# Kernel optimization log

Measured on AMD Instinct MI355X. Metric: run time of the kernel, lower is better.

The kernel has to match this reference:

```python
import jax, jax.numpy as jnp
import numpy as np

H = 256  # hidden size
I = 2    # input size / output size


def setup_inputs() -> dict:
    key = jax.random.key(0)
    ks = jax.random.split(key, 11)
    s1 = 1.0 / np.sqrt(H)
    u = lambda k, shape: jax.random.uniform(k, shape, jnp.float32, -s1, s1)
    return {
        "inputs": jax.random.normal(ks[0], (512, 256, I), jnp.float32),
        "W_ih1": u(ks[1], (4 * H, I)),
        "W_hh1": u(ks[2], (4 * H, H)),
        "b_ih1": u(ks[3], (4 * H,)),
        "b_hh1": u(ks[4], (4 * H,)),
        "W_ih2": u(ks[5], (4 * H, H)),
        "W_hh2": u(ks[6], (4 * H, H)),
        "b_ih2": u(ks[7], (4 * H,)),
        "b_hh2": u(ks[8], (4 * H,)),
        "W_lin": u(ks[9], (I, H)),
        "b_lin": u(ks[10], (I,)),
    }


def _lstm_cell(x, h, c, W_ih, W_hh, b_ih, b_hh):
    # PyTorch LSTMCell gate order: i, f, g, o
    gates = x @ W_ih.T + b_ih + h @ W_hh.T + b_hh  # (B, 4H)
    i, f, g, o = jnp.split(gates, 4, axis=-1)
    c_new = jax.nn.sigmoid(f) * c + jax.nn.sigmoid(i) * jnp.tanh(g)
    h_new = jax.nn.sigmoid(o) * jnp.tanh(c_new)
    return h_new, c_new


def reference(inputs, W_ih1, W_hh1, b_ih1, b_hh1, W_ih2, W_hh2, b_ih2, b_hh2,
              W_lin, b_lin):
    B = inputs.shape[0]
    xs = jnp.transpose(inputs, (1, 0, 2))  # (T, B, I)
    zeros = jnp.zeros((B, H), inputs.dtype)
    carry0 = (zeros, zeros, zeros, zeros)

    def step(carry, x_t):
        h1, c1, h2, c2 = carry
        # NOTE: the original clones/masks x_t into lstm_input_t but never
        # uses it — the cell consumes raw input_t, so we do the same.
        h1, c1 = _lstm_cell(x_t, h1, c1, W_ih1, W_hh1, b_ih1, b_hh1)
        h2, c2 = _lstm_cell(h1, h2, c2, W_ih2, W_hh2, b_ih2, b_hh2)
        y = h2 @ W_lin.T + b_lin  # (B, I)
        return (h1, c1, h2, c2), y

    _, ys = jax.lax.scan(step, carry0, xs)  # ys: (T, B, I)
    return jnp.transpose(ys, (1, 0, 2))  # (B, T, I)
```

## Files before the change

### kernel.cpp

```cpp
#include <hip/hip_runtime.h>


typedef float vf2 __attribute__((ext_vector_type(2)));
typedef float v4f __attribute__((ext_vector_type(4)));
typedef _Float16 vh4 __attribute__((ext_vector_type(4)));
typedef _Float16 vh8 __attribute__((ext_vector_type(8)));

#define NT 512
#define TSTEPS 256
#define NSF 160
#define NVPF 24
#define NLPF 8
#define FRB 1024
#define VPBASE (1280 * FRB)
#define LPBASE (1472 * FRB)
#define FS 393216

__global__ void prep_kernel(const float* __restrict__ W_ih1,
                            const float* __restrict__ W_hh1,
                            const float* __restrict__ b_ih1,
                            const float* __restrict__ b_hh1,
                            const float* __restrict__ W_ih2,
                            const float* __restrict__ W_hh2,
                            const float* __restrict__ b_ih2,
                            const float* __restrict__ b_hh2,
                            void* __restrict__ ws) {
    const int stride = gridDim.x * blockDim.x;
    const int idx = blockIdx.x * blockDim.x + threadIdx.x;
    _Float16* wh = (_Float16*)ws;
    float* wf = (float*)ws;
    for (int e = idx; e < 786432; e += stride) {
        int kb = e >> 9;
        int lane = (e & 511) >> 3, jj = e & 7;
        int w, rt, kt, m;
        if (kb < 1280) {
            w = kb / 160; int f = kb % 160;
            if (f < 64)       { m = 0; rt = f >> 3;        kt = f & 7; }
            else if (f < 128) { m = 1; rt = (f - 64) >> 3; kt = f & 7; }
            else {
                int q = f - 128; m = 2; rt = q >> 2; int pos = q & 3;
                kt = (pos == 0) ? 0 : (pos == 1) ? 4 : (pos == 2) ? 5 : 7;
            }
        } else if (kb < 1472) {
            int p2 = kb - 1280; w = p2 / 24; int p = p2 % 24;
            m = 2; rt = p / 3; kt = 1 + p % 3;
        } else {
            int k3 = kb - 1472; w = k3 >> 3; int q = k3 & 7;
            m = 2; rt = q; kt = 6;
        }
        int row = w * 128 + rt * 16 + (lane & 15);
        int k   = kt * 32 + ((lane >> 4) << 3) + jj;
        float v = (m == 0) ? W_hh1[row * 256 + k]
                : (m == 1) ? W_ih2[row * 256 + k]
                           : W_hh2[row * 256 + k];
        wh[e] = (_Float16)v;
    }
    for (int j = idx; j < 1024; j += stride) {
        wf[FS + j]        = W_ih1[j * 2 + 0];
        wf[FS + 1024 + j] = W_ih1[j * 2 + 1];
        wf[FS + 2048 + j] = b_ih1[j] + b_hh1[j];
        wf[FS + 3072 + j] = b_ih2[j] + b_hh2[j];
    }
}

__device__ __forceinline__ float sig_(float v) {
    return 1.f / (1.f + __expf(-v));
}
__device__ __forceinline__ float tanh_(float v) {
    return 1.f - 2.f / (__expf(2.f * v) + 1.f);
}
__device__ __forceinline__ v4f mfma16(vh8 a, vh8 b, v4f c) {
    return __builtin_amdgcn_mfma_f32_16x16x32_f16(a, b, c, 0, 0, 0);
}

#define BARRIER() __asm__ volatile("s_waitcnt lgkmcnt(0)\ns_barrier" ::: "memory")

__global__ __launch_bounds__(NT, 2) void lstm_kernel(
    const float* __restrict__ x,
    const void* __restrict__ ws,
    const float* __restrict__ W_lin,
    const float* __restrict__ b_lin,
    float* __restrict__ out)
{
    __shared__ float g1buf[2][1024];
    __shared__ float g2buf[2][1024];
    __shared__ __align__(16) _Float16 h1s[2][256];
    __shared__ __align__(16) _Float16 h2s[2][256];
    __shared__ __align__(16) char lds_park[NLPF * 8 * FRB];

    const int tid = threadIdx.x;
    const int lane = tid & 63, w = tid >> 6;
    const int u = tid & 255, bu = tid >> 8;
    const int b0 = blockIdx.x * 2;
    const char* wstream = (const char*)ws;
    const float* wf = (const float*)ws;
    const int l16 = lane * 16;

    float wxa[4], wxb[4], b1c[4], b2c[4];
    #pragma unroll
    for (int g = 0; g < 4; ++g) {
        int r = g * 256 + u;
        wxa[g] = wf[FS + r];        wxb[g] = wf[FS + 1024 + r];
        b1c[g] = wf[FS + 2048 + r]; b2c[g] = wf[FS + 3072 + r];
    }

    const int ob = (w >> 1) & 1, oo = w & 1;
    const float wl0 = W_lin[oo * 256 + 4 * lane + 0];
    const float wl1 = W_lin[oo * 256 + 4 * lane + 1];
    const float wl2 = W_lin[oo * 256 + 4 * lane + 2];
    const float wl3 = W_lin[oo * 256 + 4 * lane + 3];
    const float blin = b_lin[oo];

    ((_Float16*)h1s)[tid] = (_Float16)0.f;
    ((_Float16*)h2s)[tid] = (_Float16)0.f;
    g1buf[0][tid] = 0.f; g1buf[0][512 + tid] = 0.f;
    g1buf[1][tid] = 0.f; g1buf[1][512 + tid] = 0.f;

    float c1 = 0.f, c2 = 0.f;

    for (int q = 0; q < NLPF; ++q) {
        *(vh8*)&lds_park[(((q << 3) + w) << 10) + l16] =
            *(const vh8*)(wstream + LPBASE + (((w << 3) + q) << 10) + l16);
    }

    vh8 wreg[NVPF];
    #pragma unroll
    for (int p = 0; p < NVPF; ++p) {
        union { vh8 v; float f[4]; } tpk;
        tpk.v = *(const vh8*)(wstream + VPBASE + ((w * NVPF + p) << 10) + l16);
        asm volatile("" : "+v"(tpk.f[0]), "+v"(tpk.f[1]),
                          "+v"(tpk.f[2]), "+v"(tpk.f[3]));
        wreg[p] = tpk.v;
    }

    const char* wbase = wstream + (size_t)w * (NSF * FRB);
    int sp = 0;
    vh8 B0, B1, B2, B3, B4, B5, B6, B7, B8, B9, B10, B11, B12, B13, B14, B15;
    auto LDA = [&](vh8& d) {
        d = *(const vh8*)(wbase + sp + l16);
        sp += FRB; if (sp == NSF * FRB) sp = 0;
    };
    LDA(B0); LDA(B1); LDA(B2);  LDA(B3);  LDA(B4);  LDA(B5);  LDA(B6);  LDA(B7);
    LDA(B8); LDA(B9); LDA(B10); LDA(B11); LDA(B12); LDA(B13); LDA(B14); LDA(B15);

    auto bfrag = [&](const _Float16 (*hp)[256], int kt) -> vh8 {
        return *(const vh8*)&hp[lane & 1][kt * 32 + ((lane >> 4) << 3)];
    };

    const int bx = b0 + bu;
    vf2 xv = *(const vf2*)(x + (size_t)bx * 512);

    __syncthreads();

    #pragma unroll 1
    for (int t = 0; t < TSTEPS; ++t) {
        {
            float p0 = g1buf[bu][u]       + b1c[0] + wxa[0] * xv.x + wxb[0] * xv.y;
            float p1 = g1buf[bu][256 + u] + b1c[1] + wxa[1] * xv.x + wxb[1] * xv.y;
            float p2 = g1buf[bu][512 + u] + b1c[2] + wxa[2] * xv.x + wxb[2] * xv.y;
            float p3 = g1buf[bu][768 + u] + b1c[3] + wxa[3] * xv.x + wxb[3] * xv.y;
            c1 = sig_(p1) * c1 + sig_(p0) * tanh_(p2);
            h1s[bu][u] = (_Float16)(sig_(p3) * tanh_(c1));
        }
        {
            const int tn = (t + 1) & (TSTEPS - 1);
            xv = *(const vf2*)(x + (size_t)bx * 512 + tn * 2);
        }
        BARRIER();

        if (t > 0 && w < 4) {
            vh4 hv = *(const vh4*)&h2s[ob][4 * lane];
            float s = (float)hv.x * wl0 + (float)hv.y * wl1
                    + (float)hv.z * wl2 + (float)hv.w * wl3;
            #pragma unroll
            for (int m = 32; m >= 1; m >>= 1) s += __shfl_xor(s, m, 64);
            if (lane == 0)
                out[(size_t)(b0 + ob) * 512 + (t - 1) * 2 + oo] = s + blin;
        }

        #pragma unroll 1
        for (int rp = 0; rp < 4; ++rp) {
            v4f a0 = {0.f, 0.f, 0.f, 0.f}, a1 = {0.f, 0.f, 0.f, 0.f};
            a0 = mfma16(B0, bfrag(h1s, 0), a0); LDA(B0);
            a0 = mfma16(B1, bfrag(h1s, 1), a0); LDA(B1);
            a0 = mfma16(B2, bfrag(h1s, 2), a0); LDA(B2);
            a0 = mfma16(B3, bfrag(h1s, 3), a0); LDA(B3);
            a0 = mfma16(B4, bfrag(h1s, 4), a0); LDA(B4);
            a0 = mfma16(B5, bfrag(h1s, 5), a0); LDA(B5);
            a0 = mfma16(B6, bfrag(h1s, 6), a0); LDA(B6);
            a0 = mfma16(B7, bfrag(h1s, 7), a0); LDA(B7);
            a1 = mfma16(B8,  bfrag(h1s, 0), a1); LDA(B8);
            a1 = mfma16(B9,  bfrag(h1s, 1), a1); LDA(B9);
            a1 = mfma16(B10, bfrag(h1s, 2), a1); LDA(B10);
            a1 = mfma16(B11, bfrag(h1s, 3), a1); LDA(B11);
            a1 = mfma16(B12, bfrag(h1s, 4), a1); LDA(B12);
            a1 = mfma16(B13, bfrag(h1s, 5), a1); LDA(B13);
            a1 = mfma16(B14, bfrag(h1s, 6), a1); LDA(B14);
            a1 = mfma16(B15, bfrag(h1s, 7), a1); LDA(B15);
            if ((lane & 15) < 2) {
                *(v4f*)&g1buf[lane & 15][w * 128 + (2 * rp) * 16 + ((lane >> 4) << 2)] = a0;
                *(v4f*)&g1buf[lane & 15][w * 128 + (2 * rp + 1) * 16 + ((lane >> 4) << 2)] = a1;
            }
        }

        #pragma unroll 1
        for (int rp = 0; rp < 4; ++rp) {
            v4f a0 = {0.f, 0.f, 0.f, 0.f}, a1 = {0.f, 0.f, 0.f, 0.f};
            a0 = mfma16(B0, bfrag(h1s, 0), a0); LDA(B0);
            a0 = mfma16(B1, bfrag(h1s, 1), a0); LDA(B1);
            a0 = mfma16(B2, bfrag(h1s, 2), a0); LDA(B2);
            a0 = mfma16(B3, bfrag(h1s, 3), a0); LDA(B3);
            a0 = mfma16(B4, bfrag(h1s, 4), a0); LDA(B4);
            a0 = mfma16(B5, bfrag(h1s, 5), a0); LDA(B5);
            a0 = mfma16(B6, bfrag(h1s, 6), a0); LDA(B6);
            a0 = mfma16(B7, bfrag(h1s, 7), a0); LDA(B7);
            a1 = mfma16(B8,  bfrag(h1s, 0), a1); LDA(B8);
            a1 = mfma16(B9,  bfrag(h1s, 1), a1); LDA(B9);
            a1 = mfma16(B10, bfrag(h1s, 2), a1); LDA(B10);
            a1 = mfma16(B11, bfrag(h1s, 3), a1); LDA(B11);
            a1 = mfma16(B12, bfrag(h1s, 4), a1); LDA(B12);
            a1 = mfma16(B13, bfrag(h1s, 5), a1); LDA(B13);
            a1 = mfma16(B14, bfrag(h1s, 6), a1); LDA(B14);
            a1 = mfma16(B15, bfrag(h1s, 7), a1); LDA(B15);
            if ((lane & 15) < 2) {
                *(v4f*)&g2buf[lane & 15][w * 128 + (2 * rp) * 16 + ((lane >> 4) << 2)] = a0;
                *(v4f*)&g2buf[lane & 15][w * 128 + (2 * rp + 1) * 16 + ((lane >> 4) << 2)] = a1;
            }
        }

#define P2B(RT, BA, BB, BC, BD)                                                \
        {                                                                      \
            v4f acc = {0.f, 0.f, 0.f, 0.f};                                    \
            if ((lane & 15) < 2)                                               \
                acc = *(const v4f*)&g2buf[lane & 15]                           \
                        [w * 128 + RT * 16 + ((lane >> 4) << 2)];              \
            acc = mfma16(BA, bfrag(h2s, 0), acc); LDA(BA);                     \
            acc = mfma16(wreg[RT * 3 + 0], bfrag(h2s, 1), acc);                \
            acc = mfma16(wreg[RT * 3 + 1], bfrag(h2s, 2), acc);                \
            acc = mfma16(wreg[RT * 3 + 2], bfrag(h2s, 3), acc);                \
            acc = mfma16(BB, bfrag(h2s, 4), acc); LDA(BB);                     \
            acc = mfma16(BC, bfrag(h2s, 5), acc); LDA(BC);                     \
            {                                                                  \
                vh8 A6 = *(const vh8*)                                         \
                    &lds_park[(((RT << 3) + w) << 10) + l16];                  \
                acc = mfma16(A6, bfrag(h2s, 6), acc);                          \
            }                                                                  \
            acc = mfma16(BD, bfrag(h2s, 7), acc); LDA(BD);                     \
            if ((lane & 15) < 2)                                               \
                *(v4f*)&g2buf[lane & 15]                                       \
                    [w * 128 + RT * 16 + ((lane >> 4) << 2)] = acc;            \
        }
        P2B(0, B0,  B1,  B2,  B3)  P2B(1, B4,  B5,  B6,  B7)
        P2B(2, B8,  B9,  B10, B11) P2B(3, B12, B13, B14, B15)
        P2B(4, B0,  B1,  B2,  B3)  P2B(5, B4,  B5,  B6,  B7)
        P2B(6, B8,  B9,  B10, B11) P2B(7, B12, B13, B14, B15)
#undef P2B
        BARRIER();

        {
            float q0 = g2buf[bu][u]       + b2c[0];
            float q1 = g2buf[bu][256 + u] + b2c[1];
            float q2 = g2buf[bu][512 + u] + b2c[2];
            float q3 = g2buf[bu][768 + u] + b2c[3];
            c2 = sig_(q1) * c2 + sig_(q0) * tanh_(q2);
            h2s[bu][u] = (_Float16)(sig_(q3) * tanh_(c2));
        }
    }

    BARRIER();
    if (w < 4) {
        vh4 hv = *(const vh4*)&h2s[ob][4 * lane];
        float s = (float)hv.x * wl0 + (float)hv.y * wl1
                + (float)hv.z * wl2 + (float)hv.w * wl3;
        #pragma unroll
        for (int m = 32; m >= 1; m >>= 1) s += __shfl_xor(s, m, 64);
        if (lane == 0)
            out[(size_t)(b0 + ob) * 512 + 255 * 2 + oo] = s + blin;
    }
}

extern "C" void kernel_launch(void* const* d_in, const int* in_sizes, int n_in,
                              void* d_out, int out_size, void* d_ws, size_t ws_size,
                              hipStream_t stream) {
    const float* x     = (const float*)d_in[0];
    const float* W_ih1 = (const float*)d_in[1];
    const float* W_hh1 = (const float*)d_in[2];
    const float* b_ih1 = (const float*)d_in[3];
    const float* b_hh1 = (const float*)d_in[4];
    const float* W_ih2 = (const float*)d_in[5];
    const float* W_hh2 = (const float*)d_in[6];
    const float* b_ih2 = (const float*)d_in[7];
    const float* b_hh2 = (const float*)d_in[8];
    const float* W_lin = (const float*)d_in[9];
    const float* b_lin = (const float*)d_in[10];
    float* out = (float*)d_out;

    prep_kernel<<<256, 256, 0, stream>>>(W_ih1, W_hh1, b_ih1, b_hh1,
                                         W_ih2, W_hh2, b_ih2, b_hh2, d_ws);
    lstm_kernel<<<256, NT, 0, stream>>>(x, d_ws, W_lin, b_lin, out);
}
```

Measured before the change: 2.910 ms.

## Keep W_hh2 fully resident in AGPRs and LDS, stream fewer weight fragments

The W_hh2 fragments are now held entirely on chip: 48 fragments per wave sit in accumulation registers (AGPR constraint) and the two remaining k-tiles per row tile sit in LDS. Only W_hh1 and W_ih2 are still streamed from global memory on each step. This cuts per-step global/L2 weight traffic by 20%, at the cost of more register pressure (the AGPR file) and doubled LDS parking. The gate-1 loops are also split into separate accumulator scopes to shorten live ranges.

```diff
diff --git a/kernel.cpp b/kernel.cpp
--- a/kernel.cpp
+++ b/kernel.cpp
@@ -8,12 +8,12 @@
 
 #define NT 512
 #define TSTEPS 256
-#define NSF 160
-#define NVPF 24
-#define NLPF 8
+#define NSF 128
+#define NAPF 48
+#define NLPF 16
 #define FRB 1024
-#define VPBASE (1280 * FRB)
-#define LPBASE (1472 * FRB)
+#define ABASE (1024 * FRB)
+#define LPBASE (1408 * FRB)
 #define FS 393216
 
 __global__ void prep_kernel(const float* __restrict__ W_ih1,
@@ -33,20 +33,16 @@
         int kb = e >> 9;
         int lane = (e & 511) >> 3, jj = e & 7;
         int w, rt, kt, m;
-        if (kb < 1280) {
-            w = kb / 160; int f = kb % 160;
-            if (f < 64)       { m = 0; rt = f >> 3;        kt = f & 7; }
-            else if (f < 128) { m = 1; rt = (f - 64) >> 3; kt = f & 7; }
-            else {
-                int q = f - 128; m = 2; rt = q >> 2; int pos = q & 3;
-                kt = (pos == 0) ? 0 : (pos == 1) ? 4 : (pos == 2) ? 5 : 7;
-            }
-        } else if (kb < 1472) {
-            int p2 = kb - 1280; w = p2 / 24; int p = p2 % 24;
-            m = 2; rt = p / 3; kt = 1 + p % 3;
+        if (kb < 1024) {
+            w = kb >> 7; int f = kb & 127;
+            if (f < 64) { m = 0; rt = f >> 3;        kt = f & 7; }
+            else        { m = 1; rt = (f - 64) >> 3; kt = f & 7; }
+        } else if (kb < 1408) {
+            int p2 = kb - 1024; w = p2 / 48; int p = p2 % 48;
+            m = 2; rt = p / 6; kt = p % 6;
         } else {
-            int k3 = kb - 1472; w = k3 >> 3; int q = k3 & 7;
-            m = 2; rt = q; kt = 6;
+            int k3 = kb - 1408; w = k3 >> 4; int q = k3 & 15;
+            m = 2; rt = q >> 1; kt = 6 + (q & 1);
         }
         int row = w * 128 + rt * 16 + (lane & 15);
         int k   = kt * 32 + ((lane >> 4) << 3) + jj;
@@ -120,17 +116,17 @@
 
     for (int q = 0; q < NLPF; ++q) {
         *(vh8*)&lds_park[(((q << 3) + w) << 10) + l16] =
-            *(const vh8*)(wstream + LPBASE + (((w << 3) + q) << 10) + l16);
-    }
-
-    vh8 wreg[NVPF];
+            *(const vh8*)(wstream + LPBASE + (((w << 4) + q) << 10) + l16);
+    }
+
+    vh8 wrega[NAPF];
     #pragma unroll
-    for (int p = 0; p < NVPF; ++p) {
+    for (int p = 0; p < NAPF; ++p) {
         union { vh8 v; float f[4]; } tpk;
-        tpk.v = *(const vh8*)(wstream + VPBASE + ((w * NVPF + p) << 10) + l16);
-        asm volatile("" : "+v"(tpk.f[0]), "+v"(tpk.f[1]),
-                          "+v"(tpk.f[2]), "+v"(tpk.f[3]));
-        wreg[p] = tpk.v;
+        tpk.v = *(const vh8*)(wstream + ABASE + ((w * NAPF + p) << 10) + l16);
+        asm volatile("" : "+a"(tpk.f[0]), "+a"(tpk.f[1]),
+                          "+a"(tpk.f[2]), "+a"(tpk.f[3]));
+        wrega[p] = tpk.v;
     }
 
     const char* wbase = wstream + (size_t)w * (NSF * FRB);
@@ -180,80 +176,91 @@
 
         #pragma unroll 1
         for (int rp = 0; rp < 4; ++rp) {
-            v4f a0 = {0.f, 0.f, 0.f, 0.f}, a1 = {0.f, 0.f, 0.f, 0.f};
-            a0 = mfma16(B0, bfrag(h1s, 0), a0); LDA(B0);
-            a0 = mfma16(B1, bfrag(h1s, 1), a0); LDA(B1);
-            a0 = mfma16(B2, bfrag(h1s, 2), a0); LDA(B2);
-            a0 = mfma16(B3, bfrag(h1s, 3), a0); LDA(B3);
-            a0 = mfma16(B4, bfrag(h1s, 4), a0); LDA(B4);
-            a0 = mfma16(B5, bfrag(h1s, 5), a0); LDA(B5);
-            a0 = mfma16(B6, bfrag(h1s, 6), a0); LDA(B6);
-            a0 = mfma16(B7, bfrag(h1s, 7), a0); LDA(B7);
-            a1 = mfma16(B8,  bfrag(h1s, 0), a1); LDA(B8);
-            a1 = mfma16(B9,  bfrag(h1s, 1), a1); LDA(B9);
-            a1 = mfma16(B10, bfrag(h1s, 2), a1); LDA(B10);
-            a1 = mfma16(B11, bfrag(h1s, 3), a1); LDA(B11);
-            a1 = mfma16(B12, bfrag(h1s, 4), a1); LDA(B12);
-            a1 = mfma16(B13, bfrag(h1s, 5), a1); LDA(B13);
-            a1 = mfma16(B14, bfrag(h1s, 6), a1); LDA(B14);
-            a1 = mfma16(B15, bfrag(h1s, 7), a1); LDA(B15);
-            if ((lane & 15) < 2) {
-                *(v4f*)&g1buf[lane & 15][w * 128 + (2 * rp) * 16 + ((lane >> 4) << 2)] = a0;
-                *(v4f*)&g1buf[lane & 15][w * 128 + (2 * rp + 1) * 16 + ((lane >> 4) << 2)] = a1;
+            {
+                v4f a0 = {0.f, 0.f, 0.f, 0.f};
+                a0 = mfma16(B0, bfrag(h1s, 0), a0); LDA(B0);
+                a0 = mfma16(B1, bfrag(h1s, 1), a0); LDA(B1);
+                a0 = mfma16(B2, bfrag(h1s, 2), a0); LDA(B2);
+                a0 = mfma16(B3, bfrag(h1s, 3), a0); LDA(B3);
+                a0 = mfma16(B4, bfrag(h1s, 4), a0); LDA(B4);
+                a0 = mfma16(B5, bfrag(h1s, 5), a0); LDA(B5);
+                a0 = mfma16(B6, bfrag(h1s, 6), a0); LDA(B6);
+                a0 = mfma16(B7, bfrag(h1s, 7), a0); LDA(B7);
+                if ((lane & 15) < 2)
+                    *(v4f*)&g1buf[lane & 15][w * 128 + (2 * rp) * 16 + ((lane >> 4) << 2)] = a0;
+            }
+            {
+                v4f a1 = {0.f, 0.f, 0.f, 0.f};
+                a1 = mfma16(B8,  bfrag(h1s, 0), a1); LDA(B8);
+                a1 = mfma16(B9,  bfrag(h1s, 1), a1); LDA(B9);
+                a1 = mfma16(B10, bfrag(h1s, 2), a1); LDA(B10);
+                a1 = mfma16(B11, bfrag(h1s, 3), a1); LDA(B11);
+                a1 = mfma16(B12, bfrag(h1s, 4), a1); LDA(B12);
+                a1 = mfma16(B13, bfrag(h1s, 5), a1); LDA(B13);
+                a1 = mfma16(B14, bfrag(h1s, 6), a1); LDA(B14);
+                a1 = mfma16(B15, bfrag(h1s, 7), a1); LDA(B15);
+                if ((lane & 15) < 2)
+                    *(v4f*)&g1buf[lane & 15][w * 128 + (2 * rp + 1) * 16 + ((lane >> 4) << 2)] = a1;
             }
         }
 
         #pragma unroll 1
         for (int rp = 0; rp < 4; ++rp) {
-            v4f a0 = {0.f, 0.f, 0.f, 0.f}, a1 = {0.f, 0.f, 0.f, 0.f};
-            a0 = mfma16(B0, bfrag(h1s, 0), a0); LDA(B0);
-            a0 = mfma16(B1, bfrag(h1s, 1), a0); LDA(B1);
-            a0 = mfma16(B2, bfrag(h1s, 2), a0); LDA(B2);
-            a0 = mfma16(B3, bfrag(h1s, 3), a0); LDA(B3);
-            a0 = mfma16(B4, bfrag(h1s, 4), a0); LDA(B4);
-            a0 = mfma16(B5, bfrag(h1s, 5), a0); LDA(B5);
-            a0 = mfma16(B6, bfrag(h1s, 6), a0); LDA(B6);
-            a0 = mfma16(B7, bfrag(h1s, 7), a0); LDA(B7);
-            a1 = mfma16(B8,  bfrag(h1s, 0), a1); LDA(B8);
-            a1 = mfma16(B9,  bfrag(h1s, 1), a1); LDA(B9);
-            a1 = mfma16(B10, bfrag(h1s, 2), a1); LDA(B10);
-            a1 = mfma16(B11, bfrag(h1s, 3), a1); LDA(B11);
-            a1 = mfma16(B12, bfrag(h1s, 4), a1); LDA(B12);
-            a1 = mfma16(B13, bfrag(h1s, 5), a1); LDA(B13);
-            a1 = mfma16(B14, bfrag(h1s, 6), a1); LDA(B14);
-            a1 = mfma16(B15, bfrag(h1s, 7), a1); LDA(B15);
-            if ((lane & 15) < 2) {
-                *(v4f*)&g2buf[lane & 15][w * 128 + (2 * rp) * 16 + ((lane >> 4) << 2)] = a0;
-                *(v4f*)&g2buf[lane & 15][w * 128 + (2 * rp + 1) * 16 + ((lane >> 4) << 2)] = a1;
+            {
+                v4f a0 = {0.f, 0.f, 0.f, 0.f};
+                a0 = mfma16(B0, bfrag(h1s, 0), a0); LDA(B0);
+                a0 = mfma16(B1, bfrag(h1s, 1), a0); LDA(B1);
+                a0 = mfma16(B2, bfrag(h1s, 2), a0); LDA(B2);
+                a0 = mfma16(B3, bfrag(h1s, 3), a0); LDA(B3);
+                a0 = mfma16(B4, bfrag(h1s, 4), a0); LDA(B4);
+                a0 = mfma16(B5, bfrag(h1s, 5), a0); LDA(B5);
+                a0 = mfma16(B6, bfrag(h1s, 6), a0); LDA(B6);
+                a0 = mfma16(B7, bfrag(h1s, 7), a0); LDA(B7);
+                if ((lane & 15) < 2)
+                    *(v4f*)&g2buf[lane & 15][w * 128 + (2 * rp) * 16 + ((lane >> 4) << 2)] = a0;
             }
-        }
-
-#define P2B(RT, BA, BB, BC, BD)                                                \
+            {
+                v4f a1 = {0.f, 0.f, 0.f, 0.f};
+                a1 = mfma16(B8,  bfrag(h1s, 0), a1); LDA(B8);
+                a1 = mfma16(B9,  bfrag(h1s, 1), a1); LDA(B9);
+                a1 = mfma16(B10, bfrag(h1s, 2), a1); LDA(B10);
+                a1 = mfma16(B11, bfrag(h1s, 3), a1); LDA(B11);
+                a1 = mfma16(B12, bfrag(h1s, 4), a1); LDA(B12);
+                a1 = mfma16(B13, bfrag(h1s, 5), a1); LDA(B13);
+                a1 = mfma16(B14, bfrag(h1s, 6), a1); LDA(B14);
+                a1 = mfma16(B15, bfrag(h1s, 7), a1); LDA(B15);
+                if ((lane & 15) < 2)
+                    *(v4f*)&g2buf[lane & 15][w * 128 + (2 * rp + 1) * 16 + ((lane >> 4) << 2)] = a1;
+            }
+        }
+
+#define P2B(RT)                                                                \
         {                                                                      \
             v4f acc = {0.f, 0.f, 0.f, 0.f};                                    \
             if ((lane & 15) < 2)                                               \
                 acc = *(const v4f*)&g2buf[lane & 15]                           \
                         [w * 128 + RT * 16 + ((lane >> 4) << 2)];              \
-            acc = mfma16(BA, bfrag(h2s, 0), acc); LDA(BA);                     \
-            acc = mfma16(wreg[RT * 3 + 0], bfrag(h2s, 1), acc);                \
-            acc = mfma16(wreg[RT * 3 + 1], bfrag(h2s, 2), acc);                \
-            acc = mfma16(wreg[RT * 3 + 2], bfrag(h2s, 3), acc);                \
-            acc = mfma16(BB, bfrag(h2s, 4), acc); LDA(BB);                     \
-            acc = mfma16(BC, bfrag(h2s, 5), acc); LDA(BC);                     \
+            acc = mfma16(wrega[RT * 6 + 0], bfrag(h2s, 0), acc);               \
+            acc = mfma16(wrega[RT * 6 + 1], bfrag(h2s, 1), acc);               \
+            acc = mfma16(wrega[RT * 6 + 2], bfrag(h2s, 2), acc);               \
+            acc = mfma16(wrega[RT * 6 + 3], bfrag(h2s, 3), acc);               \
+            acc = mfma16(wrega[RT * 6 + 4], bfrag(h2s, 4), acc);               \
+            acc = mfma16(wrega[RT * 6 + 5], bfrag(h2s, 5), acc);               \
             {                                                                  \
                 vh8 A6 = *(const vh8*)                                         \
-                    &lds_park[(((RT << 3) + w) << 10) + l16];                  \
+                    &lds_park[((((RT * 2 + 0) << 3) + w) << 10) + l16];        \
                 acc = mfma16(A6, bfrag(h2s, 6), acc);                          \
             }                                                                  \
-            acc = mfma16(BD, bfrag(h2s, 7), acc); LDA(BD);                     \
+            {                                                                  \
+                vh8 A7 = *(const vh8*)                                         \
+                    &lds_park[((((RT * 2 + 1) << 3) + w) << 10) + l16];        \
+                acc = mfma16(A7, bfrag(h2s, 7), acc);                          \
+            }                                                                  \
             if ((lane & 15) < 2)                                               \
                 *(v4f*)&g2buf[lane & 15]                                       \
                     [w * 128 + RT * 16 + ((lane >> 4) << 2)] = acc;            \
         }
-        P2B(0, B0,  B1,  B2,  B3)  P2B(1, B4,  B5,  B6,  B7)
-        P2B(2, B8,  B9,  B10, B11) P2B(3, B12, B13, B14, B15)
-        P2B(4, B0,  B1,  B2,  B3)  P2B(5, B4,  B5,  B6,  B7)
-        P2B(6, B8,  B9,  B10, B11) P2B(7, B12, B13, B14, B15)
+        P2B(0) P2B(1) P2B(2) P2B(3) P2B(4) P2B(5) P2B(6) P2B(7)
 #undef P2B
         BARRIER();
 
```

Result: slower. 5.124 ms (+76.1%).
